# Kernel tuning notes

Hardware: AMD Instinct MI355X
Metric: run time of the kernel (lower is better)

Reference implementation:

```python
import jax, jax.numpy as jnp
import numpy as np

DIM = 384
DH = 32
H = DIM // DH          # 12 heads
N_WIN = 3072           # total windows
W_ACT = 1536           # active windows = M
T = 64                 # tokens per window (8x8)
NTOK = W_ACT * T       # 98304 active tokens
N_BLOCK = 9830
MLP = 4 * DIM
EPS = 1e-5


def _layer_norm(h, w, b):
    mu = jnp.mean(h, axis=-1, keepdims=True)
    var = jnp.mean(jnp.square(h - mu), axis=-1, keepdims=True)
    return (h - mu) * jax.lax.rsqrt(var + EPS) * w + b


def setup_inputs() -> dict:
    key = jax.random.key(0)
    ks = jax.random.split(key, 16)
    x = jax.random.normal(ks[0], (N_WIN, T, DIM), jnp.float32)
    # unique active windows, sorted (scatter-restore requires uniqueness)
    index_window = jnp.sort(jax.random.permutation(ks[1], N_WIN)[:W_ACT])
    # full permutation of active tokens into M groups of size S
    index_partition = jax.random.permutation(ks[2], NTOK)
    blocked_index = jax.random.permutation(ks[3], NTOK)[:N_BLOCK]
    s = 0.02
    params = dict(
        ln1_w=jnp.ones((DIM,), jnp.float32), ln1_b=jnp.zeros((DIM,), jnp.float32),
        qkv_w=jax.random.normal(ks[4], (3 * DIM, DIM), jnp.float32) * s,
        qkv_b=jnp.zeros((3 * DIM,), jnp.float32),
        proj_w=jax.random.normal(ks[5], (DIM, DIM), jnp.float32) * s,
        proj_b=jnp.zeros((DIM,), jnp.float32),
        ln2_w=jnp.ones((DIM,), jnp.float32), ln2_b=jnp.zeros((DIM,), jnp.float32),
        fc1_w=jax.random.normal(ks[6], (MLP, DIM), jnp.float32) * s,
        fc1_b=jnp.zeros((MLP,), jnp.float32),
        fc2_w=jax.random.normal(ks[7], (DIM, MLP), jnp.float32) * s,
        fc2_b=jnp.zeros((DIM,), jnp.float32),
    )
    return dict(x=x, index_window=index_window, index_partition=index_partition,
                blocked_index=blocked_index, M=W_ACT, K=jnp.zeros((1,), jnp.int64),
                **params)


def reference(x, index_window, index_partition, blocked_index, M, K,
              ln1_w, ln1_b, qkv_w, qkv_b, proj_w, proj_b,
              ln2_w, ln2_b, fc1_w, fc1_b, fc2_w, fc2_b):
    N, T_, C = x.shape
    scale = DH ** -0.5
    S = index_partition.shape[0] // M

    xn = _layer_norm(x, ln1_w, ln1_b)                      # (N, T, C)
    xw = xn[index_window].reshape(-1, C)                   # (NTOK, C) active tokens
    xp = xw[index_partition].reshape(M, S, C)              # (M, S, C) regrouped
    shortcut = xp

    qkv = (xp @ qkv_w.T + qkv_b).reshape(M, S, H, 3 * DH)  # per-head [q|k|v] chunks
    q, k, v = qkv[..., :DH], qkv[..., DH:2 * DH], qkv[..., 2 * DH:]

    attn = jnp.einsum('mqhd,mkhd->mhqk', q, k) * scale     # (M, H, Sq, Sk)

    # scatter scores into full-size map keyed by KEY token, mask blocked keys, gather back
    amap = jnp.zeros((xw.shape[0], S, H), attn.dtype)      # (NTOK, Sq, H)
    amap = amap.at[index_partition].set(jnp.transpose(attn, (0, 3, 2, 1)).reshape(-1, S, H))
    amap = amap.at[blocked_index].set(-10000.0)
    attn = jnp.transpose(amap[index_partition].reshape(M, S, S, H), (0, 3, 2, 1))
    attn = jax.nn.softmax(attn, axis=-1)

    o = jnp.einsum('mhqk,mkhd->mqhd', attn, v).reshape(M, S, C)
    o = o @ proj_w.T + proj_b

    # sub_layers: [Id, Id(+res), LN, fc1, GELU, fc2(+res)]
    h = shortcut + o
    shortcut = h
    h2 = _layer_norm(h, ln2_w, ln2_b)
    h2 = jax.nn.gelu(h2 @ fc1_w.T + fc1_b, approximate=False)
    h = shortcut + (h2 @ fc2_w.T + fc2_b)

    # scatter-restore: blocked tokens keep their (normed) input values
    XX = xw.at[index_partition].set(h.reshape(-1, C))
    XX = XX.at[blocked_index].set(xw[blocked_index])
    out = xn.at[index_window].set(XX.reshape(M, -1, C))
    return out
```

## Files before the change

kernel.cpp:

```cpp
#include <hip/hip_runtime.h>
#include <hip/hip_bf16.h>

typedef __attribute__((ext_vector_type(8))) short bf16x8;
typedef __attribute__((ext_vector_type(4))) short s16x4;
typedef __attribute__((ext_vector_type(4))) float f32x4;
typedef __attribute__((ext_vector_type(2))) long longx2;
typedef __attribute__((ext_vector_type(16))) unsigned char u8x16;

#define NW_   3072
#define WACT_ 1536
#define NTOK_ 98304
#define NBLK_ 9830
#define DIM_  384
#define QKVD_ 1152
#define MLPD_ 1536

__device__ __forceinline__ float bf2f(short s) {
  union { unsigned u; float f; } c;
  c.u = ((unsigned)(unsigned short)s) << 16;
  return c.f;
}
__device__ __forceinline__ short f2bf(float f) {
  union { float f; unsigned u; } c; c.f = f;
  unsigned lsb = (c.u >> 16) & 1u;
  c.u += 0x7fffu + lsb;
  return (short)(c.u >> 16);
}

__device__ __forceinline__ f32x4 mfma16(bf16x8 a, bf16x8 b, f32x4 c) {
  return __builtin_amdgcn_mfma_f32_16x16x32_bf16(a, b, c, 0, 0, 0);
}
__device__ __forceinline__ f32x4 mfma8(long a, long b, f32x4 c) {
  return __builtin_amdgcn_mfma_f32_16x16x32_fp8_fp8(a, b, c, 0, 0, 0);
}

__device__ __forceinline__ void gload16(const void* g, void* l) {
  __builtin_amdgcn_global_load_lds(
      (const __attribute__((address_space(1))) unsigned*)g,
      (__attribute__((address_space(3))) unsigned*)l, 16, 0, 0);
}

__device__ __forceinline__ int kperm(int col) {
  int l = (col >> 3) & 7;
  int s = ((l & 3) << 1) | (l >> 2);
  return (col & ~63) + s * 8 + (col & 7);
}

__global__ __launch_bounds__(256) void mapA_k(int* win_rank, unsigned* bitmap) {
  int t = blockIdx.x * 256 + threadIdx.x;
  if (t < NW_) { win_rank[t] = -1; bitmap[t] = 0u; }
}

__global__ __launch_bounds__(256) void mapB_k(const int* __restrict__ iw,
                                              const int* __restrict__ blk,
                                              int* win_rank, unsigned* bitmap) {
  int t = blockIdx.x * 256 + threadIdx.x;
  if (t < WACT_) win_rank[iw[t]] = t;
  if (t < NBLK_) { int j = blk[t]; atomicOr(&bitmap[j >> 5], 1u << (j & 31)); }
}

__global__ __launch_bounds__(256) void mapC_k(const int* __restrict__ ip,
                                              const int* __restrict__ iw,
                                              const unsigned* __restrict__ bitmap,
                                              int* inv_ip, int* rowmap) {
  int i = blockIdx.x * 256 + threadIdx.x;
  if (i < NTOK_) {
    int j = ip[i];
    inv_ip[j] = i;
    int blocked = (bitmap[j >> 5] >> (j & 31)) & 1;
    rowmap[i] = blocked ? -1 : (iw[j >> 6] * 64 + (j & 63));
  }
}

__global__ __launch_bounds__(256) void wconv_k(const float* __restrict__ qkvw,
                                               short* __restrict__ dst) {
  int i = (blockIdx.x * 256 + threadIdx.x) * 4;
  f32x4 v = *(const f32x4*)&qkvw[i];
  s16x4 o;
#pragma unroll
  for (int e = 0; e < 4; ++e) o[e] = f2bf(v[e]);
  *(s16x4*)&dst[i] = o;
}

__global__ __launch_bounds__(256) void wconv8_k(const float* __restrict__ src,
                                                unsigned char* __restrict__ dst,
                                                int K) {
  int i = (blockIdx.x * 256 + threadIdx.x) * 8;
  f32x4 v0 = *(const f32x4*)&src[i];
  f32x4 v1 = *(const f32x4*)&src[i + 4];
  int w0 = __builtin_amdgcn_cvt_pk_fp8_f32(v0[0], v0[1], 0, false);
  w0 = __builtin_amdgcn_cvt_pk_fp8_f32(v0[2], v0[3], w0, true);
  int w1 = __builtin_amdgcn_cvt_pk_fp8_f32(v1[0], v1[1], 0, false);
  w1 = __builtin_amdgcn_cvt_pk_fp8_f32(v1[2], v1[3], w1, true);
  int kro = i % K, row = i / K;
  union { int u[2]; long ll; } p; p.u[0] = w0; p.u[1] = w1;
  *(long*)&dst[(size_t)row * K + kperm(kro)] = p.ll;
}

__global__ __launch_bounds__(256) void ln1_k(const float* __restrict__ x,
                                             const float* __restrict__ w,
                                             const float* __restrict__ b,
                                             const int* __restrict__ win_rank,
                                             const int* __restrict__ inv_ip,
                                             const unsigned* __restrict__ bitmap,
                                             float* __restrict__ out,
                                             short* __restrict__ xp) {
  const int l = threadIdx.x & 31;
  const int tok = blockIdx.x * 8 + (threadIdx.x >> 5);
  const f32x4* xr = (const f32x4*)(x + (size_t)tok * DIM_);
  f32x4 v[3]; float s = 0.f;
#pragma unroll
  for (int j = 0; j < 3; ++j) {
    v[j] = xr[l + 32 * j];
    s += v[j][0] + v[j][1] + v[j][2] + v[j][3];
  }
#pragma unroll
  for (int m = 1; m <= 16; m <<= 1) s += __shfl_xor(s, m, 64);
  float mu = s * (1.0f / DIM_);
  float q = 0.f;
#pragma unroll
  for (int j = 0; j < 3; ++j)
#pragma unroll
    for (int e = 0; e < 4; ++e) { float d = v[j][e] - mu; q += d * d; }
#pragma unroll
  for (int m = 1; m <= 16; m <<= 1) q += __shfl_xor(q, m, 64);
  float rs = rsqrtf(q * (1.0f / DIM_) + 1e-5f);
  f32x4 y[3];
#pragma unroll
  for (int j = 0; j < 3; ++j) {
    f32x4 wv = *(const f32x4*)&w[4 * l + 128 * j];
    f32x4 bv = *(const f32x4*)&b[4 * l + 128 * j];
#pragma unroll
    for (int e = 0; e < 4; ++e) y[j][e] = (v[j][e] - mu) * rs * wv[e] + bv[e];
  }
  int wdw = tok >> 6, t = tok & 63;
  int rank = win_rank[wdw];
  if (rank < 0) {
    f32x4* po = (f32x4*)(out + (size_t)tok * DIM_);
#pragma unroll
    for (int j = 0; j < 3; ++j) po[l + 32 * j] = y[j];
  } else {
    int jdx = (rank << 6) + t;
    int i = inv_ip[jdx];
#pragma unroll
    for (int j = 0; j < 3; ++j) {
      s16x4 o;
#pragma unroll
      for (int e = 0; e < 4; ++e) o[e] = f2bf(y[j][e]);
      *(s16x4*)&xp[(size_t)i * DIM_ + 4 * l + 128 * j] = o;
    }
    if ((bitmap[jdx >> 5] >> (jdx & 31)) & 1) {
      f32x4* po = (f32x4*)(out + (size_t)tok * DIM_);
#pragma unroll
      for (int j = 0; j < 3; ++j) po[l + 32 * j] = y[j];
    }
  }
}

__global__ __launch_bounds__(256) void ln2_k(const short* __restrict__ h,
                                             const float* __restrict__ w,
                                             const float* __restrict__ b,
                                             unsigned char* __restrict__ out8) {
  const int l = threadIdx.x & 31;
  const int tok = blockIdx.x * 8 + (threadIdx.x >> 5);
  const s16x4* xr = (const s16x4*)(h + (size_t)tok * DIM_);
  float v[12]; float s = 0.f;
#pragma unroll
  for (int j = 0; j < 3; ++j) {
    s16x4 rv = xr[l + 32 * j];
#pragma unroll
    for (int e = 0; e < 4; ++e) { v[j * 4 + e] = bf2f(rv[e]); s += v[j * 4 + e]; }
  }
#pragma unroll
  for (int m = 1; m <= 16; m <<= 1) s += __shfl_xor(s, m, 64);
  float mu = s * (1.0f / DIM_);
  float q = 0.f;
#pragma unroll
  for (int e = 0; e < 12; ++e) { float d = v[e] - mu; q += d * d; }
#pragma unroll
  for (int m = 1; m <= 16; m <<= 1) q += __shfl_xor(q, m, 64);
  float rs = rsqrtf(q * (1.0f / DIM_) + 1e-5f);
#pragma unroll
  for (int j = 0; j < 3; ++j) {
    f32x4 wv = *(const f32x4*)&w[4 * l + 128 * j];
    f32x4 bv = *(const f32x4*)&b[4 * l + 128 * j];
    float y[4];
#pragma unroll
    for (int e = 0; e < 4; ++e)
      y[e] = (v[j * 4 + e] - mu) * rs * wv[e] + bv[e];
    int wrd = __builtin_amdgcn_cvt_pk_fp8_f32(y[0], y[1], 0, false);
    wrd = __builtin_amdgcn_cvt_pk_fp8_f32(y[2], y[3], wrd, true);
    int c0 = 4 * l + 128 * j;
    *(unsigned*)&out8[(size_t)tok * DIM_ + kperm(c0)] = (unsigned)wrd;
  }
}

__global__ __launch_bounds__(512) void gemmqkv_k(const short* __restrict__ A,
                                                 const short* __restrict__ B,
                                                 const float* __restrict__ bias,
                                                 unsigned char* __restrict__ C8) {
  const int K = 384, N = QKVD_, nx = 9;
  const int nwg = gridDim.x;
  const int q8 = nwg >> 3;
  const int wg = (blockIdx.x & 7) * q8 + (blockIdx.x >> 3);
  const int ntile = wg % nx, mtile = wg / nx;
  const int tid = threadIdx.x, wid = tid >> 6, lane = tid & 63;
  const int fq = lane >> 4, fr = lane & 15;
  const int wr = wid >> 1, wc = wid & 1;
  __shared__ __align__(16) short lA[256 * 64];
  __shared__ __align__(16) short lB[128 * 64];
  const int row0 = mtile * 256, col0 = ntile * 128;
  float bs[4];
#pragma unroll
  for (int nt = 0; nt < 4; ++nt) bs[nt] = bias[col0 + wc * 64 + nt * 16 + fr];
  f32x4 acc[4][4];
#pragma unroll
  for (int a = 0; a < 4; ++a)
#pragma unroll
    for (int c = 0; c < 4; ++c) acc[a][c] = (f32x4){0.f, 0.f, 0.f, 0.f};
  const int nkt = K >> 6;
  for (int kt = 0; kt < nkt; ++kt) {
    const int k0 = kt << 6;
#pragma unroll
    for (int i = 0; i < 4; ++i) {
      int g = i * 512 + tid;
      int r = g >> 3, c8 = g & 7;
      int s8 = c8 ^ (r & 7);
      gload16(A + (size_t)(row0 + r) * K + k0 + s8 * 8, (char*)lA + (size_t)g * 16);
    }
#pragma unroll
    for (int i = 0; i < 2; ++i) {
      int g = i * 512 + tid;
      int r = g >> 3, c8 = g & 7;
      int s8 = c8 ^ (r & 7);
      gload16(B + (size_t)(col0 + r) * K + k0 + s8 * 8, (char*)lB + (size_t)g * 16);
    }
    __syncthreads();
#pragma unroll
    for (int ks = 0; ks < 2; ++ks) {
      bf16x8 af[4], bfr[4];
#pragma unroll
      for (int mt = 0; mt < 4; ++mt) {
        int r = wr * 64 + mt * 16 + fr;
        af[mt] = *(const bf16x8*)&lA[r * 64 + ((ks * 4 + fq) ^ (r & 7)) * 8];
      }
#pragma unroll
      for (int nt = 0; nt < 4; ++nt) {
        int r = wc * 64 + nt * 16 + fr;
        bfr[nt] = *(const bf16x8*)&lB[r * 64 + ((ks * 4 + fq) ^ (r & 7)) * 8];
      }
#pragma unroll
      for (int mt = 0; mt < 4; ++mt)
#pragma unroll
        for (int nt = 0; nt < 4; ++nt)
          acc[mt][nt] = mfma16(af[mt], bfr[nt], acc[mt][nt]);
    }
    __syncthreads();
  }
#pragma unroll
  for (int mt = 0; mt < 4; ++mt) {
#pragma unroll
    for (int jj = 0; jj < 4; ++jj) {
      int r = row0 + wr * 64 + mt * 16 + fq * 4 + jj;
      float g4[4];
#pragma unroll
      for (int nt = 0; nt < 4; ++nt) g4[nt] = acc[mt][nt][jj] + bs[nt];
      int p01 = __builtin_amdgcn_cvt_pk_fp8_f32(g4[0], g4[1], 0, false);
      int p23 = __builtin_amdgcn_cvt_pk_fp8_f32(g4[2], g4[3], 0, false);
      const size_t rb = (size_t)r * N + col0 + wc * 64 + fr;
      C8[rb]      = (unsigned char)(p01 & 0xff);
      C8[rb + 16] = (unsigned char)((p01 >> 8) & 0xff);
      C8[rb + 32] = (unsigned char)(p23 & 0xff);
      C8[rb + 48] = (unsigned char)((p23 >> 8) & 0xff);
    }
  }
}

template <int EPI>
__global__ __launch_bounds__(256) void gemmf8_k(const unsigned char* __restrict__ A8,
                                                const unsigned char* __restrict__ B8,
                                                const float* __restrict__ bias,
                                                int K, int nx,
                                                short* __restrict__ Cb,
                                                unsigned char* __restrict__ C8,
                                                const short* __restrict__ add_bf,
                                                const int* __restrict__ rowmap,
                                                float* __restrict__ outf) {
  const int nwg = gridDim.x;
  const int q8 = nwg >> 3;
  const int wg = (blockIdx.x & 7) * q8 + (blockIdx.x >> 3);
  const int ntile = wg % nx, mtile = wg / nx;
  const int tid = threadIdx.x, wid = tid >> 6, lane = tid & 63;
  const int fq = lane >> 4, fr = lane & 15;
  const int wr = wid >> 1, wc = wid & 1;
  __shared__ __align__(16) unsigned char lA[128 * 128];
  __shared__ __align__(16) unsigned char lB[128 * 128];
  const int row0 = mtile * 128, col0 = ntile * 128;
  float bs[4];
#pragma unroll
  for (int nt = 0; nt < 4; ++nt) bs[nt] = bias[col0 + wc * 64 + nt * 16 + fr];
  f32x4 acc[4][4];
#pragma unroll
  for (int a = 0; a < 4; ++a)
#pragma unroll
    for (int c = 0; c < 4; ++c) acc[a][c] = (f32x4){0.f, 0.f, 0.f, 0.f};
  const int nkt = K >> 7;
  for (int kt = 0; kt < nkt; ++kt) {
    const int k0 = kt << 7;
#pragma unroll
    for (int i = 0; i < 4; ++i) {
      int g = i * 256 + tid;
      int r = g >> 3, c8 = g & 7;
      int s8 = c8 ^ (r & 7);
      gload16(A8 + (size_t)(row0 + r) * K + k0 + s8 * 16, (char*)lA + (size_t)g * 16);
      gload16(B8 + (size_t)(col0 + r) * K + k0 + s8 * 16, (char*)lB + (size_t)g * 16);
    }
    __syncthreads();
#pragma unroll
    for (int ss = 0; ss < 2; ++ss) {
      longx2 af[4], bfr[4];
      const int pb = ss * 4 + fq;
#pragma unroll
      for (int mt = 0; mt < 4; ++mt) {
        int r = wr * 64 + mt * 16 + fr;
        int d = pb ^ (r & 7);
        af[mt] = *(const longx2*)&lA[r * 128 + d * 16];
      }
#pragma unroll
      for (int nt = 0; nt < 4; ++nt) {
        int r = wc * 64 + nt * 16 + fr;
        int d = pb ^ (r & 7);
        bfr[nt] = *(const longx2*)&lB[r * 128 + d * 16];
      }
#pragma unroll
      for (int mt = 0; mt < 4; ++mt)
#pragma unroll
        for (int nt = 0; nt < 4; ++nt) {
          acc[mt][nt] = mfma8(af[mt][0], bfr[nt][0], acc[mt][nt]);
          acc[mt][nt] = mfma8(af[mt][1], bfr[nt][1], acc[mt][nt]);
        }
    }
    __syncthreads();
  }
#pragma unroll
  for (int mt = 0; mt < 4; ++mt) {
#pragma unroll
    for (int jj = 0; jj < 4; ++jj) {
      int r = row0 + wr * 64 + mt * 16 + fq * 4 + jj;
      int dmap = 0;
      if (EPI == 3) dmap = rowmap[r];
      if (EPI == 1) {
#pragma unroll
        for (int nt = 0; nt < 4; ++nt) {
          int gcol = col0 + wc * 64 + nt * 16 + fr;
          float v = acc[mt][nt][jj] + bs[nt] + bf2f(add_bf[(size_t)r * DIM_ + gcol]);
          Cb[(size_t)r * DIM_ + gcol] = f2bf(v);
        }
      } else if (EPI == 2) {
        float g4[4];
#pragma unroll
        for (int nt = 0; nt < 4; ++nt) {
          float v = acc[mt][nt][jj] + bs[nt];
          float u = v * (0.79788456f + 0.03567741f * v * v);
          g4[nt] = v * __builtin_amdgcn_rcpf(1.0f + __expf(-2.0f * u));
        }
        int p01 = __builtin_amdgcn_cvt_pk_fp8_f32(g4[0], g4[1], 0, false);
        int p23 = __builtin_amdgcn_cvt_pk_fp8_f32(g4[2], g4[3], 0, false);
        const int C0 = col0 + wc * 64;
        const size_t rb = (size_t)r * MLPD_ + C0 + (fr & 7) + ((fr >> 3) << 4);
        C8[rb]      = (unsigned char)(p01 & 0xff);
        C8[rb + 32] = (unsigned char)((p01 >> 8) & 0xff);
        C8[rb + 8]  = (unsigned char)(p23 & 0xff);
        C8[rb + 40] = (unsigned char)((p23 >> 8) & 0xff);
      } else {
#pragma unroll
        for (int nt = 0; nt < 4; ++nt) {
          int gcol = col0 + wc * 64 + nt * 16 + fr;
          float v = acc[mt][nt][jj] + bs[nt] + bf2f(add_bf[(size_t)r * DIM_ + gcol]);
          if (dmap >= 0) outf[(size_t)dmap * DIM_ + gcol] = v;
        }
      }
    }
  }
}

__global__ __launch_bounds__(256) void attn_k(const unsigned char* __restrict__ qkv8,
                                              const unsigned* __restrict__ bitmap,
                                              const int* __restrict__ ip,
                                              unsigned char* __restrict__ o8) {
  const int flat = (blockIdx.x & 7) * 576 + (blockIdx.x >> 3);
  const int m = flat / 3;
  const int h = (flat % 3) * 4 + (threadIdx.x >> 6);
  const int wid = threadIdx.x >> 6, lane = threadIdx.x & 63;
  const int fq = lane >> 4, fr = lane & 15;
  __shared__ __align__(16) unsigned char P[4][64 * 72];
  __shared__ __align__(16) unsigned char Vt[4][32 * 72];
  __shared__ unsigned char flags[64];
  if (threadIdx.x < 64) {
    int j = ip[m * 64 + threadIdx.x];
    flags[threadIdx.x] = (unsigned char)((bitmap[j >> 5] >> (j & 31)) & 1);
  }
  __syncthreads();
  const float scale = 0.17677669529663687f;
  int msk[4];
#pragma unroll
  for (int nt = 0; nt < 4; ++nt) msk[nt] = flags[nt * 16 + fr];

  const unsigned char* base = qkv8 + (size_t)m * 64 * QKVD_ + h * 96;
  f32x4 sacc[4][4];
#pragma unroll
  for (int a = 0; a < 4; ++a)
#pragma unroll
    for (int c = 0; c < 4; ++c) sacc[a][c] = (f32x4){0.f, 0.f, 0.f, 0.f};
  long qa[4], kb[4];
#pragma unroll
  for (int mt = 0; mt < 4; ++mt)
    qa[mt] = *(const long*)(base + (size_t)(mt * 16 + fr) * QKVD_ + fq * 8);
#pragma unroll
  for (int nt = 0; nt < 4; ++nt)
    kb[nt] = *(const long*)(base + (size_t)(nt * 16 + fr) * QKVD_ + 32 + fq * 8);
#pragma unroll
  for (int mt = 0; mt < 4; ++mt)
#pragma unroll
    for (int nt = 0; nt < 4; ++nt)
      sacc[mt][nt] = mfma8(qa[mt], kb[nt], sacc[mt][nt]);
#pragma unroll
  for (int c = 0; c < 2; ++c) {
    u8x16 vv = *(const u8x16*)(base + (size_t)lane * QKVD_ + 64 + c * 16);
#pragma unroll
    for (int e = 0; e < 16; ++e) Vt[wid][(c * 16 + e) * 72 + lane] = vv[e];
  }
#pragma unroll
  for (int mt = 0; mt < 4; ++mt)
#pragma unroll
    for (int nt = 0; nt < 4; ++nt) {
      f32x4 sv = sacc[mt][nt];
#pragma unroll
      for (int jj = 0; jj < 4; ++jj)
        sv[jj] = msk[nt] ? -10000.0f : sv[jj] * scale;
      sacc[mt][nt] = sv;
    }
#pragma unroll
  for (int mt = 0; mt < 4; ++mt) {
#pragma unroll
    for (int jj = 0; jj < 4; ++jj) {
      float mx = sacc[mt][0][jj];
#pragma unroll
      for (int nt = 1; nt < 4; ++nt) mx = fmaxf(mx, sacc[mt][nt][jj]);
#pragma unroll
      for (int mm = 1; mm < 16; mm <<= 1) mx = fmaxf(mx, __shfl_xor(mx, mm, 64));
      float sm = 0.f;
      float p[4];
#pragma unroll
      for (int nt = 0; nt < 4; ++nt) {
        p[nt] = __expf(sacc[mt][nt][jj] - mx);
        sm += p[nt];
      }
#pragma unroll
      for (int mm = 1; mm < 16; mm <<= 1) sm += __shfl_xor(sm, mm, 64);
      float inv = 1.0f / sm;
      int rowb = (mt * 16 + fq * 4 + jj) * 72;
      int p01 = __builtin_amdgcn_cvt_pk_fp8_f32(p[0] * inv, p[1] * inv, 0, false);
      int p23 = __builtin_amdgcn_cvt_pk_fp8_f32(p[2] * inv, p[3] * inv, 0, false);
      P[wid][rowb + fr]      = (unsigned char)(p01 & 0xff);
      P[wid][rowb + 16 + fr] = (unsigned char)((p01 >> 8) & 0xff);
      P[wid][rowb + 32 + fr] = (unsigned char)(p23 & 0xff);
      P[wid][rowb + 48 + fr] = (unsigned char)((p23 >> 8) & 0xff);
    }
  }
  f32x4 oacc[4][2];
#pragma unroll
  for (int a = 0; a < 4; ++a)
#pragma unroll
    for (int c = 0; c < 2; ++c) oacc[a][c] = (f32x4){0.f, 0.f, 0.f, 0.f};
#pragma unroll
  for (int ks = 0; ks < 2; ++ks) {
    long pa[4], vb[2];
#pragma unroll
    for (int mt = 0; mt < 4; ++mt)
      pa[mt] = *(const long*)&P[wid][(mt * 16 + fr) * 72 + ks * 32 + fq * 8];
#pragma unroll
    for (int nd = 0; nd < 2; ++nd)
      vb[nd] = *(const long*)&Vt[wid][(nd * 16 + fr) * 72 + ks * 32 + fq * 8];
#pragma unroll
    for (int mt = 0; mt < 4; ++mt)
#pragma unroll
      for (int nd = 0; nd < 2; ++nd)
        oacc[mt][nd] = mfma8(pa[mt], vb[nd], oacc[mt][nd]);
  }
  const int pos0 = kperm(h * 32 + fr);
  const int pos1 = kperm(h * 32 + 16 + fr);
#pragma unroll
  for (int mt = 0; mt < 4; ++mt)
#pragma unroll
    for (int jj = 0; jj < 4; ++jj) {
      int p01 = __builtin_amdgcn_cvt_pk_fp8_f32(oacc[mt][0][jj], oacc[mt][1][jj],
                                                0, false);
      size_t rb = (size_t)(m * 64 + mt * 16 + fq * 4 + jj) * DIM_;
      o8[rb + pos0] = (unsigned char)(p01 & 0xff);
      o8[rb + pos1] = (unsigned char)((p01 >> 8) & 0xff);
    }
}

extern "C" void kernel_launch(void* const* d_in, const int* in_sizes, int n_in,
                              void* d_out, int out_size, void* d_ws, size_t ws_size,
                              hipStream_t stream) {
  const float* x = (const float*)d_in[0];
  const int* iw = (const int*)d_in[1];
  const int* ip = (const int*)d_in[2];
  const int* blk = (const int*)d_in[3];
  const float* ln1w = (const float*)d_in[6];
  const float* ln1b = (const float*)d_in[7];
  const float* qkvw = (const float*)d_in[8];
  const float* qkvb = (const float*)d_in[9];
  const float* projw = (const float*)d_in[10];
  const float* projb = (const float*)d_in[11];
  const float* ln2w = (const float*)d_in[12];
  const float* ln2b = (const float*)d_in[13];
  const float* fc1w = (const float*)d_in[14];
  const float* fc1b = (const float*)d_in[15];
  const float* fc2w = (const float*)d_in[16];
  const float* fc2b = (const float*)d_in[17];
  float* out = (float*)d_out;

  char* ws = (char*)d_ws;
  short* w_qkv = (short*)ws;
  unsigned char* projw8 = (unsigned char*)(ws + 884736);
  unsigned char* fc1w8 = (unsigned char*)(ws + 1032192);
  unsigned char* fc2w8 = (unsigned char*)(ws + 1622016);
  int* inv_ip = (int*)(ws + 2211840);
  int* rowmap = inv_ip + NTOK_;
  int* win_rank = rowmap + NTOK_;
  unsigned* bitmap = (unsigned*)(win_rank + NW_);
  short* xp = (short*)(ws + 4349952);
  unsigned char* qkv8 = (unsigned char*)(ws + 79847424);
  unsigned char* t8 = qkv8;
  unsigned char* obuf8 = (unsigned char*)(ws + 306339840);
  unsigned char* ln2buf8 = (unsigned char*)(ws + 344088576);
  short* hbuf = (short*)(ws + 457334784);
  (void)in_sizes; (void)n_in; (void)out_size; (void)ws_size;

  mapA_k<<<12, 256, 0, stream>>>(win_rank, bitmap);
  mapB_k<<<39, 256, 0, stream>>>(iw, blk, win_rank, bitmap);
  mapC_k<<<NTOK_ / 256, 256, 0, stream>>>(ip, iw, bitmap, inv_ip, rowmap);
  wconv_k<<<432, 256, 0, stream>>>(qkvw, w_qkv);
  wconv8_k<<<72, 256, 0, stream>>>(projw, projw8, 384);
  wconv8_k<<<288, 256, 0, stream>>>(fc1w, fc1w8, 384);
  wconv8_k<<<288, 256, 0, stream>>>(fc2w, fc2w8, MLPD_);
  ln1_k<<<(NW_ * 64) / 8, 256, 0, stream>>>(x, ln1w, ln1b, win_rank, inv_ip, bitmap,
                                            out, xp);
  gemmqkv_k<<<384 * 9, 512, 0, stream>>>(xp, w_qkv, qkvb, qkv8);
  attn_k<<<WACT_ * 3, 256, 0, stream>>>(qkv8, bitmap, ip, obuf8);
  gemmf8_k<1><<<768 * 3, 256, 0, stream>>>(obuf8, projw8, projb, 384, 3, hbuf,
                                           nullptr, xp, nullptr, nullptr);
  ln2_k<<<NTOK_ / 8, 256, 0, stream>>>(hbuf, ln2w, ln2b, ln2buf8);
  gemmf8_k<2><<<768 * 12, 256, 0, stream>>>(ln2buf8, fc1w8, fc1b, 384, 12, nullptr,
                                            t8, nullptr, nullptr, nullptr);
  gemmf8_k<3><<<768 * 3, 256, 0, stream>>>(t8, fc2w8, fc2b, MLPD_, 3, nullptr,
                                           nullptr, hbuf, rowmap, out);
}
```

Measured before the change: 704.0 us.

## Enlarge fp8 GEMM tile to 256 rows and merge weight prep kernels

Merges the map-init and four weight-conversion kernels into one multi-role launch to cut launch overhead. It also grows the fp8 GEMM tile from 128x128 to 256x128, using 512 threads and eight waves, so each B tile loaded into LDS feeds twice as many rows. This halves the grid size and raises LDS use per workgroup to 48 KB, which may lower occupancy. The wave-role mapping (wr = wid>>1) now spans 4 row groups, consistent with 256 rows.

New measurement: 623.1 us. 11.5% less time.

```diff
diff --git a/kernel.cpp b/kernel.cpp
--- a/kernel.cpp
+++ b/kernel.cpp
@@ -46,9 +46,48 @@
   return (col & ~63) + s * 8 + (col & 7);
 }
 
-__global__ __launch_bounds__(256) void mapA_k(int* win_rank, unsigned* bitmap) {
-  int t = blockIdx.x * 256 + threadIdx.x;
-  if (t < NW_) { win_rank[t] = -1; bitmap[t] = 0u; }
+__device__ __forceinline__ void conv8_chunk(const float* __restrict__ src,
+                                            unsigned char* __restrict__ dst,
+                                            int K, int blk, int tid) {
+  int i = (blk * 256 + tid) * 8;
+  f32x4 v0 = *(const f32x4*)&src[i];
+  f32x4 v1 = *(const f32x4*)&src[i + 4];
+  int w0 = __builtin_amdgcn_cvt_pk_fp8_f32(v0[0], v0[1], 0, false);
+  w0 = __builtin_amdgcn_cvt_pk_fp8_f32(v0[2], v0[3], w0, true);
+  int w1 = __builtin_amdgcn_cvt_pk_fp8_f32(v1[0], v1[1], 0, false);
+  w1 = __builtin_amdgcn_cvt_pk_fp8_f32(v1[2], v1[3], w1, true);
+  int kro = i % K, row = i / K;
+  union { int u[2]; long ll; } p; p.u[0] = w0; p.u[1] = w1;
+  *(long*)&dst[(size_t)row * K + kperm(kro)] = p.ll;
+}
+
+__global__ __launch_bounds__(256) void pre_k(const float* __restrict__ qkvw,
+                                             const float* __restrict__ projw,
+                                             const float* __restrict__ fc1w,
+                                             const float* __restrict__ fc2w,
+                                             short* __restrict__ wq,
+                                             unsigned char* __restrict__ pw8,
+                                             unsigned char* __restrict__ f1w8,
+                                             unsigned char* __restrict__ f2w8,
+                                             int* win_rank, unsigned* bitmap) {
+  const int bid = blockIdx.x, tid = threadIdx.x;
+  if (bid < 12) {
+    int t = bid * 256 + tid;
+    if (t < NW_) { win_rank[t] = -1; bitmap[t] = 0u; }
+  } else if (bid < 444) {
+    int i = ((bid - 12) * 256 + tid) * 4;
+    f32x4 v = *(const f32x4*)&qkvw[i];
+    s16x4 o;
+#pragma unroll
+    for (int e = 0; e < 4; ++e) o[e] = f2bf(v[e]);
+    *(s16x4*)&wq[i] = o;
+  } else if (bid < 516) {
+    conv8_chunk(projw, pw8, 384, bid - 444, tid);
+  } else if (bid < 804) {
+    conv8_chunk(fc1w, f1w8, 384, bid - 516, tid);
+  } else {
+    conv8_chunk(fc2w, f2w8, MLPD_, bid - 804, tid);
+  }
 }
 
 __global__ __launch_bounds__(256) void mapB_k(const int* __restrict__ iw,
@@ -70,31 +109,6 @@
     int blocked = (bitmap[j >> 5] >> (j & 31)) & 1;
     rowmap[i] = blocked ? -1 : (iw[j >> 6] * 64 + (j & 63));
   }
-}
-
-__global__ __launch_bounds__(256) void wconv_k(const float* __restrict__ qkvw,
-                                               short* __restrict__ dst) {
-  int i = (blockIdx.x * 256 + threadIdx.x) * 4;
-  f32x4 v = *(const f32x4*)&qkvw[i];
-  s16x4 o;
-#pragma unroll
-  for (int e = 0; e < 4; ++e) o[e] = f2bf(v[e]);
-  *(s16x4*)&dst[i] = o;
-}
-
-__global__ __launch_bounds__(256) void wconv8_k(const float* __restrict__ src,
-                                                unsigned char* __restrict__ dst,
-                                                int K) {
-  int i = (blockIdx.x * 256 + threadIdx.x) * 8;
-  f32x4 v0 = *(const f32x4*)&src[i];
-  f32x4 v1 = *(const f32x4*)&src[i + 4];
-  int w0 = __builtin_amdgcn_cvt_pk_fp8_f32(v0[0], v0[1], 0, false);
-  w0 = __builtin_amdgcn_cvt_pk_fp8_f32(v0[2], v0[3], w0, true);
-  int w1 = __builtin_amdgcn_cvt_pk_fp8_f32(v1[0], v1[1], 0, false);
-  w1 = __builtin_amdgcn_cvt_pk_fp8_f32(v1[2], v1[3], w1, true);
-  int kro = i % K, row = i / K;
-  union { int u[2]; long ll; } p; p.u[0] = w0; p.u[1] = w1;
-  *(long*)&dst[(size_t)row * K + kperm(kro)] = p.ll;
 }
 
 __global__ __launch_bounds__(256) void ln1_k(const float* __restrict__ x,
@@ -277,7 +291,7 @@
 }
 
 template <int EPI>
-__global__ __launch_bounds__(256) void gemmf8_k(const unsigned char* __restrict__ A8,
+__global__ __launch_bounds__(512) void gemmf8_k(const unsigned char* __restrict__ A8,
                                                 const unsigned char* __restrict__ B8,
                                                 const float* __restrict__ bias,
                                                 int K, int nx,
@@ -293,9 +307,9 @@
   const int tid = threadIdx.x, wid = tid >> 6, lane = tid & 63;
   const int fq = lane >> 4, fr = lane & 15;
   const int wr = wid >> 1, wc = wid & 1;
-  __shared__ __align__(16) unsigned char lA[128 * 128];
+  __shared__ __align__(16) unsigned char lA[256 * 128];
   __shared__ __align__(16) unsigned char lB[128 * 128];
-  const int row0 = mtile * 128, col0 = ntile * 128;
+  const int row0 = mtile * 256, col0 = ntile * 128;
   float bs[4];
 #pragma unroll
   for (int nt = 0; nt < 4; ++nt) bs[nt] = bias[col0 + wc * 64 + nt * 16 + fr];
@@ -309,10 +323,16 @@
     const int k0 = kt << 7;
 #pragma unroll
     for (int i = 0; i < 4; ++i) {
-      int g = i * 256 + tid;
+      int g = i * 512 + tid;
       int r = g >> 3, c8 = g & 7;
       int s8 = c8 ^ (r & 7);
       gload16(A8 + (size_t)(row0 + r) * K + k0 + s8 * 16, (char*)lA + (size_t)g * 16);
+    }
+#pragma unroll
+    for (int i = 0; i < 2; ++i) {
+      int g = i * 512 + tid;
+      int r = g >> 3, c8 = g & 7;
+      int s8 = c8 ^ (r & 7);
       gload16(B8 + (size_t)(col0 + r) * K + k0 + s8 * 16, (char*)lB + (size_t)g * 16);
     }
     __syncthreads();
@@ -540,22 +560,19 @@
   short* hbuf = (short*)(ws + 457334784);
   (void)in_sizes; (void)n_in; (void)out_size; (void)ws_size;
 
-  mapA_k<<<12, 256, 0, stream>>>(win_rank, bitmap);
+  pre_k<<<1092, 256, 0, stream>>>(qkvw, projw, fc1w, fc2w, w_qkv, projw8, fc1w8,
+                                  fc2w8, win_rank, bitmap);
   mapB_k<<<39, 256, 0, stream>>>(iw, blk, win_rank, bitmap);
   mapC_k<<<NTOK_ / 256, 256, 0, stream>>>(ip, iw, bitmap, inv_ip, rowmap);
-  wconv_k<<<432, 256, 0, stream>>>(qkvw, w_qkv);
-  wconv8_k<<<72, 256, 0, stream>>>(projw, projw8, 384);
-  wconv8_k<<<288, 256, 0, stream>>>(fc1w, fc1w8, 384);
-  wconv8_k<<<288, 256, 0, stream>>>(fc2w, fc2w8, MLPD_);
   ln1_k<<<(NW_ * 64) / 8, 256, 0, stream>>>(x, ln1w, ln1b, win_rank, inv_ip, bitmap,
                                             out, xp);
   gemmqkv_k<<<384 * 9, 512, 0, stream>>>(xp, w_qkv, qkvb, qkv8);
   attn_k<<<WACT_ * 3, 256, 0, stream>>>(qkv8, bitmap, ip, obuf8);
-  gemmf8_k<1><<<768 * 3, 256, 0, stream>>>(obuf8, projw8, projb, 384, 3, hbuf,
+  gemmf8_k<1><<<384 * 3, 512, 0, stream>>>(obuf8, projw8, projb, 384, 3, hbuf,
                                            nullptr, xp, nullptr, nullptr);
   ln2_k<<<NTOK_ / 8, 256, 0, stream>>>(hbuf, ln2w, ln2b, ln2buf8);
-  gemmf8_k<2><<<768 * 12, 256, 0, stream>>>(ln2buf8, fc1w8, fc1b, 384, 12, nullptr,
+  gemmf8_k<2><<<384 * 12, 512, 0, stream>>>(ln2buf8, fc1w8, fc1b, 384, 12, nullptr,
                                             t8, nullptr, nullptr, nullptr);
-  gemmf8_k<3><<<768 * 3, 256, 0, stream>>>(t8, fc2w8, fc2b, MLPD_, 3, nullptr,
+  gemmf8_k<3><<<384 * 3, 512, 0, stream>>>(t8, fc2w8, fc2b, MLPD_, 3, nullptr,
                                            nullptr, hbuf, rowmap, out);
 }
```
